# Kernel optimization log

Measured on AMD Instinct MI355X. Metric: run time of the kernel, lower is better.

Reference implementation:

```python
import jax, jax.numpy as jnp
import numpy as np

INV_SQRT2 = 0.7071067811865476


def _quadrature_ops(d):
    # truncated harmonic-oscillator ladder operator: a[n, n+1] = sqrt(n+1)
    a = jnp.diag(jnp.sqrt(jnp.arange(1, d, dtype=jnp.float32)), k=1)
    X0 = (a + a.T) * INV_SQRT2
    P0 = (a - a.T) * INV_SQRT2  # real-valued stand-in for the momentum quadrature
    I = jnp.eye(d, dtype=jnp.float32)
    return I, X0, P0


def setup_inputs() -> dict:
    key = jax.random.key(0)
    ks = jax.random.split(key, 6)
    D, d, w, K = 512, 32, 8, 4
    return {
        "mps_params": jax.random.normal(ks[0], (D, d, D), dtype=jnp.float32),
        "theta": jax.random.normal(ks[1], (1,), dtype=jnp.float32),
        "env_L": jax.random.normal(ks[2], (K, D, w, D), dtype=jnp.float32) * 0.1,
        "env_R": jax.random.normal(ks[3], (K, D, w, D), dtype=jnp.float32) * 0.1,
        "coeffs": jax.random.normal(ks[4], (K, w, w, 5), dtype=jnp.float32),
        "prefactors": jax.random.normal(ks[5], (K,), dtype=jnp.float32),
    }


def reference(mps_params, theta, env_L, env_R, coeffs, prefactors):
    A = mps_params  # [D(left), d(phys), D(right)]
    d = A.shape[1]
    K = prefactors.shape[0]

    # norm_fn: psi.H @ psi for a single-tensor MPS is sum(A^2)
    An = A / jnp.sqrt(jnp.sum(A * A))

    # _get_XandP: quadrature rotation from basis params
    I, X0, P0 = _quadrature_ops(d)
    c, s = jnp.cos(theta[0]), jnp.sin(theta[0])
    X = c * X0 + s * P0
    P = -s * X0 + c * P0

    # dynamic MPO cores: W_k[i,j] = sum_c coeffs[k,i,j,c] * ops[c]
    ops = jnp.stack([I, X, P, X @ X, P @ P])  # [5, d, d]
    W = jnp.einsum('kijc,cab->kijab', coeffs, ops)  # [K, w, w, d, d]

    out = jnp.zeros((), dtype=A.dtype)
    for k in range(K):  # fixed small loop over Hamiltonian constituents
        # T: [L, w, p, r]
        T = jnp.einsum('Lwl,lpr->Lwpr', env_L[k], An)
        # apply MPO core: [L, v, P, r]
        T = jnp.einsum('wvPp,Lwpr->LvPr', W[k], T)
        # close with right env: [L, P, R]
        T = jnp.einsum('LvPr,Rvr->LPR', T, env_R[k])
        out = out + prefactors[k] * jnp.einsum('LPR,LPR->', An, T)
    return out
```

## Files before the change

kernel.cpp:

```cpp
#include <hip/hip_runtime.h>


typedef __attribute__((ext_vector_type(8))) _Float16 f16x8;
typedef __attribute__((ext_vector_type(4))) float f32x4;

__device__ __forceinline__ unsigned short f2h(float f) {
    _Float16 h = (_Float16)f;
    return *(unsigned short*)&h;
}

__device__ __forceinline__ void gload16(const void* g, void* l) {
    __builtin_amdgcn_global_load_lds(
        (const __attribute__((address_space(1))) void*)g,
        (__attribute__((address_space(3))) void*)l, 16, 0, 0);
}

struct GArg {
    const unsigned short* A;
    const unsigned short* B;
    unsigned short* C;
    int kshift;
    long long kextra;
};

__device__ __forceinline__ void stage_tile(
    const GArg& g, int row0, int col0, int kt0,
    short* dstA, short* dstB, int tid)
{
    #pragma unroll
    for (int q = 0; q < 4; ++q) {
        const int c = q * 512 + tid;
        const int r = c >> 3;
        const int gs = (c & 7) ^ (r & 7);
        const int gr = row0 + r;
        const size_t aoff = (size_t)gr * 512 + (size_t)((unsigned)gr >> g.kshift) * g.kextra;
        gload16(g.A + aoff + kt0 + gs * 8, dstA + c * 8);
        gload16(g.B + (size_t)(col0 + r) * 512 + kt0 + gs * 8, dstB + c * 8);
    }
}

__global__ __launch_bounds__(512, 2) void gemm_dual256(int K, GArg g0, GArg g1)
{
    __shared__ short lds[65536];
    const GArg g = blockIdx.z ? g1 : g0;
    const int tid = threadIdx.x;
    const int wid = tid >> 6, lane = tid & 63;
    const int wm = wid >> 2, wn = wid & 3;
    const int lrow = lane & 15, lgrp = lane >> 4;
    const int sx = lrow & 7;
    const int gsw0 = (lgrp ^ sx) * 8, gsw1 = ((lgrp + 4) ^ sx) * 8;

    const int flat = blockIdx.y * 64 + blockIdx.x;
    const int xcd = flat & 7, local = flat >> 3;
    const int col0 = (xcd * 8 + (local & 7)) * 256;
    const int row0 = (local >> 3) * 256;

    const int nt = K >> 6;
    short* A0 = lds;          short* B0 = lds + 16384;
    short* A1 = lds + 32768;  short* B1 = lds + 49152;

    f32x4 acc[8][4] = {};

    stage_tile(g, row0, col0, 0, A0, B0, tid);
    stage_tile(g, row0, col0, 64, A1, B1, tid);
    asm volatile("s_waitcnt vmcnt(8)" ::: "memory");
    __builtin_amdgcn_s_barrier();
    __builtin_amdgcn_sched_barrier(0);

    for (int t = 0; t < nt; ++t) {
        const short* cA = (t & 1) ? A1 : A0;
        const short* cB = (t & 1) ? B1 : B0;
        short* wA = (t & 1) ? A1 : A0;
        short* wB = (t & 1) ? B1 : B0;

        f16x8 bfr[4][2], afr[4][2];
        #pragma unroll
        for (int j = 0; j < 4; ++j) {
            const int R = wn * 64 + j * 16 + lrow;
            bfr[j][0] = *(const f16x8*)&cB[R * 64 + gsw0];
            bfr[j][1] = *(const f16x8*)&cB[R * 64 + gsw1];
        }
        #pragma unroll
        for (int i = 0; i < 4; ++i) {
            const int R = wm * 128 + i * 16 + lrow;
            afr[i][0] = *(const f16x8*)&cA[R * 64 + gsw0];
            afr[i][1] = *(const f16x8*)&cA[R * 64 + gsw1];
        }
        __builtin_amdgcn_s_setprio(1);
        #pragma unroll
        for (int i = 0; i < 4; ++i)
            #pragma unroll
            for (int j = 0; j < 4; ++j) {
                acc[i][j] = __builtin_amdgcn_mfma_f32_16x16x32_f16(afr[i][0], bfr[j][0], acc[i][j], 0, 0, 0);
                acc[i][j] = __builtin_amdgcn_mfma_f32_16x16x32_f16(afr[i][1], bfr[j][1], acc[i][j], 0, 0, 0);
            }
        __builtin_amdgcn_s_setprio(0);
        #pragma unroll
        for (int i = 0; i < 4; ++i) {
            const int R = wm * 128 + (i + 4) * 16 + lrow;
            afr[i][0] = *(const f16x8*)&cA[R * 64 + gsw0];
            afr[i][1] = *(const f16x8*)&cA[R * 64 + gsw1];
        }
        asm volatile("s_waitcnt lgkmcnt(0)" ::: "memory");
        __builtin_amdgcn_sched_barrier(0);
        __builtin_amdgcn_s_barrier();
        __builtin_amdgcn_sched_barrier(0);
        if (t + 2 < nt)
            stage_tile(g, row0, col0, (t + 2) * 64, wA, wB, tid);
        __builtin_amdgcn_s_setprio(1);
        #pragma unroll
        for (int i = 0; i < 4; ++i)
            #pragma unroll
            for (int j = 0; j < 4; ++j) {
                acc[i + 4][j] = __builtin_amdgcn_mfma_f32_16x16x32_f16(afr[i][0], bfr[j][0], acc[i + 4][j], 0, 0, 0);
                acc[i + 4][j] = __builtin_amdgcn_mfma_f32_16x16x32_f16(afr[i][1], bfr[j][1], acc[i + 4][j], 0, 0, 0);
            }
        __builtin_amdgcn_s_setprio(0);
        if (t < nt - 1) {
            if (t + 2 < nt) asm volatile("s_waitcnt vmcnt(8)" ::: "memory");
            else            asm volatile("s_waitcnt vmcnt(0)" ::: "memory");
            __builtin_amdgcn_sched_barrier(0);
            __builtin_amdgcn_s_barrier();
            __builtin_amdgcn_sched_barrier(0);
        }
    }

    const int orow = lgrp * 4, ocol = lrow;
    __syncthreads();
    #pragma unroll
    for (int h = 0; h < 2; ++h) {
        if (wm == h) {
            #pragma unroll
            for (int i = 0; i < 8; ++i)
                #pragma unroll
                for (int j = 0; j < 4; ++j)
                    #pragma unroll
                    for (int q = 0; q < 4; ++q)
                        lds[(i * 16 + orow + q) * 264 + wn * 64 + j * 16 + ocol] =
                            (short)f2h(acc[i][j][q]);
        }
        __syncthreads();
        #pragma unroll
        for (int s2 = 0; s2 < 8; ++s2) {
            const int ch = s2 * 512 + tid;
            const int rr = ch >> 5, c16 = ch & 31;
            *(int4*)(g.C + (size_t)(row0 + h * 128 + rr) * 16384 + col0 + c16 * 8) =
                *(const int4*)&lds[rr * 264 + c16 * 8];
        }
        __syncthreads();
    }
}

__global__ __launch_bounds__(1024) void gemm_g4w(
    const unsigned short* __restrict__ T1, const unsigned short* __restrict__ Yp,
    const float* __restrict__ W2p, float* __restrict__ dacc,
    int Lt8, int zkShift, int BKC)
{
    __shared__ short sh[16384];
    const int tid = threadIdx.x;
    const int wid = tid >> 6, lane = tid & 63;
    const int kidx = blockIdx.x >> zkShift;
    const int kz = (blockIdx.x - (kidx << zkShift)) * BKC;
    const int wr = (wid >> 2) * 64, wc = (wid & 3) * 64;
    const int lrow = lane & 15, kb = (lane >> 4) * 8;

    const int r = tid >> 2, kc = (tid & 3) * 8;
    const int w_ = r >> 5, p_ = r & 31;
    const size_t T1k = (size_t)kidx * Lt8 * 16384;
    const size_t Yk = (size_t)kidx * 4096;
    const size_t aoff = T1k + (size_t)w_ * 16384 + (size_t)p_ * 512;
    const size_t boff = Yk + (size_t)p_ * 16384 + (size_t)w_ * 512;

    f32x4 acc[4][4] = {};

    for (int k0 = 0; k0 < BKC; k0 += 32) {
        const int kk = kz + k0;
        const int lt = kk >> 9, rbase = kk & 511;
        gload16(T1 + aoff + (size_t)lt * 131072 + rbase + kc, sh + tid * 8);
        gload16(Yp + boff + (size_t)lt * 524288 + rbase + kc, sh + 8192 + tid * 8);
        __syncthreads();
        f16x8 a[4], b[4];
        #pragma unroll
        for (int i = 0; i < 4; ++i)
            a[i] = *(const f16x8*)&sh[(wr + i * 16 + lrow) * 32 + kb];
        #pragma unroll
        for (int j = 0; j < 4; ++j)
            b[j] = *(const f16x8*)&sh[8192 + (wc + j * 16 + lrow) * 32 + kb];
        #pragma unroll
        for (int i = 0; i < 4; ++i)
            #pragma unroll
            for (int j = 0; j < 4; ++j)
                acc[i][j] = __builtin_amdgcn_mfma_f32_16x16x32_f16(a[i], b[j], acc[i][j], 0, 0, 0);
        __syncthreads();
    }

    const int orow = (lane >> 4) * 4, ocol = lane & 15;
    const float* Wk = W2p + ((size_t)kidx << 16);
    float s = 0.f;
    #pragma unroll
    for (int j = 0; j < 4; ++j) {
        const int n = wc + j * 16 + ocol;
        const float* wrow = Wk + (size_t)n * 256 + wr + orow;
        #pragma unroll
        for (int i = 0; i < 4; ++i) {
            float4 wv = *(const float4*)(wrow + i * 16);
            s += wv.x * acc[i][j][0] + wv.y * acc[i][j][1]
               + wv.z * acc[i][j][2] + wv.w * acc[i][j][3];
        }
    }
    __syncthreads();
    float* red = (float*)sh;
    red[tid] = s;
    __syncthreads();
    for (int st = 512; st > 0; st >>= 1) {
        if (tid < st) red[tid] += red[tid + st];
        __syncthreads();
    }
    if (tid == 0) atomicAdd(dacc, red[0]);
}

__global__ __launch_bounds__(256) void cast_sumsq(
    const float* __restrict__ in, unsigned short* __restrict__ out,
    long long n4, float* __restrict__ sumsq)
{
    float p = 0.f;
    for (long long i = (long long)blockIdx.x * blockDim.x + threadIdx.x; i < n4;
         i += (long long)gridDim.x * blockDim.x) {
        float4 v = ((const float4*)in)[i];
        p += v.x * v.x + v.y * v.y + v.z * v.z + v.w * v.w;
        union { unsigned short s[4]; uint2 d; } o;
        o.s[0] = f2h(v.x); o.s[1] = f2h(v.y); o.s[2] = f2h(v.z); o.s[3] = f2h(v.w);
        ((uint2*)out)[i] = o.d;
    }
    __shared__ float sh[256];
    sh[threadIdx.x] = p;
    __syncthreads();
    for (int s = 128; s > 0; s >>= 1) {
        if (threadIdx.x < s) sh[threadIdx.x] += sh[threadIdx.x + s];
        __syncthreads();
    }
    if (threadIdx.x == 0) atomicAdd(sumsq, sh[0]);
}

__global__ void cast_kernel(const float* __restrict__ in, unsigned short* __restrict__ out,
                            long long n4)
{
    for (long long i = (long long)blockIdx.x * blockDim.x + threadIdx.x; i < n4;
         i += (long long)gridDim.x * blockDim.x) {
        float4 v = ((const float4*)in)[i];
        union { unsigned short s[4]; uint2 d; } o;
        o.s[0] = f2h(v.x); o.s[1] = f2h(v.y); o.s[2] = f2h(v.z); o.s[3] = f2h(v.w);
        ((uint2*)out)[i] = o.d;
    }
}

__global__ void transpose_cast(const float* __restrict__ in, unsigned short* __restrict__ out,
                               int R, int C, long long in_stride, long long out_stride)
{
    __shared__ float tile[32][33];
    in += (long long)blockIdx.z * in_stride;
    out += (long long)blockIdx.z * out_stride;
    int c0 = blockIdx.x * 32, r0 = blockIdx.y * 32;
    int tx = threadIdx.x, ty = threadIdx.y;
    #pragma unroll
    for (int i = 0; i < 4; ++i)
        tile[ty + i * 8][tx] = in[(size_t)(r0 + ty + i * 8) * C + c0 + tx];
    __syncthreads();
    #pragma unroll
    for (int i = 0; i < 4; ++i)
        out[(size_t)(c0 + ty + i * 8) * R + r0 + tx] = f2h(tile[tx][ty + i * 8]);
}

__global__ void build_ops(const float* __restrict__ theta, float* __restrict__ ops)
{
    __shared__ float X[32][32], Pm[32][32];
    int i = threadIdx.y, j = threadIdx.x;
    float c = cosf(theta[0]), s = sinf(theta[0]);
    float aij = (j == i + 1) ? sqrtf((float)j) : 0.f;
    float aji = (i == j + 1) ? sqrtf((float)i) : 0.f;
    const float inv = 0.70710678118654752440f;
    float x0 = (aij + aji) * inv;
    float p0 = (aij - aji) * inv;
    X[i][j] = c * x0 + s * p0;
    Pm[i][j] = -s * x0 + c * p0;
    __syncthreads();
    float xx = 0.f, pp = 0.f;
    #pragma unroll
    for (int m = 0; m < 32; ++m) {
        xx += X[i][m] * X[m][j];
        pp += Pm[i][m] * Pm[m][j];
    }
    ops[0 * 1024 + i * 32 + j] = (i == j) ? 1.f : 0.f;
    ops[1 * 1024 + i * 32 + j] = X[i][j];
    ops[2 * 1024 + i * 32 + j] = Pm[i][j];
    ops[3 * 1024 + i * 32 + j] = xx;
    ops[4 * 1024 + i * 32 + j] = pp;
}

__global__ void build_w(const float* __restrict__ coeffs, const float* __restrict__ ops,
                        const float* __restrict__ pref, float* __restrict__ W2)
{
    int b = blockIdx.x;
    int k = b >> 6, w = (b >> 3) & 7, v = b & 7;
    int P = threadIdx.y, p = threadIdx.x;
    const float* cf = coeffs + ((k * 8 + w) * 8 + v) * 5;
    float acc = 0.f;
    #pragma unroll
    for (int c = 0; c < 5; ++c) acc += cf[c] * ops[c * 1024 + P * 32 + p];
    W2[(size_t)k * 65536 + (v * 32 + P) * 256 + (w * 32 + p)] = acc * pref[k];
}

__global__ void finalize_kernel(const float* __restrict__ dacc, const float* __restrict__ sumsq,
                                float* __restrict__ out)
{
    if (threadIdx.x == 0) out[0] = dacc[0] / sumsq[0];
}

extern "C" void kernel_launch(void* const* d_in, const int* in_sizes, int n_in,
                              void* d_out, int out_size, void* d_ws, size_t ws_size,
                              hipStream_t stream)
{
    const float* A      = (const float*)d_in[0];
    const float* theta  = (const float*)d_in[1];
    const float* envL   = (const float*)d_in[2];
    const float* envR   = (const float*)d_in[3];
    const float* coeffs = (const float*)d_in[4];
    const float* pref   = (const float*)d_in[5];
    float* out = (float*)d_out;

    char* ws = (char*)d_ws;
    float* sumsq = (float*)ws;
    float* dacc  = (float*)(ws + 4);
    float* ops   = (float*)(ws + 64);
    float* W2    = (float*)(ws + (32 << 10));
    unsigned short* envLh  = (unsigned short*)(ws + (4ull << 20));
    unsigned short* Ah     = (unsigned short*)(ws + (21ull << 20));
    unsigned short* Ath    = (unsigned short*)(ws + (38ull << 20));
    unsigned short* envRth = (unsigned short*)(ws + (55ull << 20));
    const size_t big0 = 72ull << 20;

    int Lt = 64;
    while (Lt > 8) {
        size_t need = big0 + 2ull * (size_t)Lt * (1ull << 20);
        if (need <= ws_size) break;
        Lt >>= 1;
    }
    unsigned short* T1 = (unsigned short*)(ws + big0);
    unsigned short* Yp = T1 + (size_t)Lt * 524288;

    const int Lt8 = Lt * 8;
    const int kshiftA = __builtin_ctz(Lt8);
    const long long kextraA = 2097152LL - (long long)Lt8 * 512;
    const int KT = Lt * 512;
    int BKC = KT / 64; if (BKC < 128) BKC = 128;
    const int zk = KT / BKC;
    const int zkShift = __builtin_ctz(zk);

    hipMemsetAsync(ws, 0, 64, stream);

    cast_sumsq<<<1024, 256, 0, stream>>>(A, Ah, 2097152LL, sumsq);
    build_ops<<<1, dim3(32, 32), 0, stream>>>(theta, ops);
    build_w<<<256, dim3(32, 32), 0, stream>>>(coeffs, ops, pref, W2);
    cast_kernel<<<2048, 256, 0, stream>>>(envL, envLh, 2097152LL);
    transpose_cast<<<dim3(512, 16, 1), dim3(32, 8), 0, stream>>>(A, Ath, 512, 16384, 0, 0);
    transpose_cast<<<dim3(128, 16, 4), dim3(32, 8), 0, stream>>>(envR, envRth, 512, 4096,
                                                                 2097152LL, 2097152LL);

    const int ntiles = 512 / Lt;
    for (int t = 0; t < ntiles; ++t) {
        GArg g0, g1;
        g0.A = envLh + (size_t)t * Lt8 * 512; g0.B = Ath; g0.C = T1;
        g0.kshift = kshiftA; g0.kextra = kextraA;
        g1.A = Ah + (size_t)t * Lt * 16384; g1.B = envRth; g1.C = Yp;
        g1.kshift = 30; g1.kextra = 0;
        gemm_dual256<<<dim3(64, (Lt * 32) / 256, 2), 512, 0, stream>>>(512, g0, g1);
        gemm_g4w<<<dim3(4 * zk), 1024, 0, stream>>>(T1, Yp, W2, dacc, Lt8, zkShift, BKC);
    }
    finalize_kernel<<<1, 64, 0, stream>>>(dacc, sumsq, out);
}
```

Before: 1.042 ms.

## Split GEMM K-tile into half-slabs with four-phase interleaved load/MFMA pipeline

Restructures the 256x256 GEMM main loop so each 64-wide K tile is stored as two 32-wide half-slabs per operand. Global-to-LDS loads are issued in quarter-sized chunks between four MFMA phases, each separated by barriers, instead of one bulk stage per tile. The LDS swizzle changes to match the 32-wide slab layout. Launch bounds drop from 2 to 1 block per CU, which allows more registers but reduces occupancy, and the extra barriers per tile add synchronisation cost.

Result: slower. 1.080 ms (+3.7%).

```diff
diff --git a/kernel.cpp b/kernel.cpp
--- a/kernel.cpp
+++ b/kernel.cpp
@@ -23,23 +23,54 @@
     long long kextra;
 };
 
-__device__ __forceinline__ void stage_tile(
-    const GArg& g, int row0, int col0, int kt0,
-    short* dstA, short* dstB, int tid)
-{
-    #pragma unroll
-    for (int q = 0; q < 4; ++q) {
-        const int c = q * 512 + tid;
-        const int r = c >> 3;
-        const int gs = (c & 7) ^ (r & 7);
-        const int gr = row0 + r;
-        const size_t aoff = (size_t)gr * 512 + (size_t)((unsigned)gr >> g.kshift) * g.kextra;
-        gload16(g.A + aoff + kt0 + gs * 8, dstA + c * 8);
-        gload16(g.B + (size_t)(col0 + r) * 512 + kt0 + gs * 8, dstB + c * 8);
-    }
-}
-
-__global__ __launch_bounds__(512, 2) void gemm_dual256(int K, GArg g0, GArg g1)
+__device__ __forceinline__ void stage_half(
+    const GArg& g, short* lds, int row0, int col0, int tid,
+    int tt, int kh, int isB)
+{
+    short* dst = lds + (tt & 1) * 32768 + isB * 16384 + kh * 8192;
+    const unsigned short* src = isB ? g.B : g.A;
+    #pragma unroll
+    for (int q = 0; q < 2; ++q) {
+        const int s = q * 512 + tid;
+        const int row = s >> 2;
+        const int kgs = (s & 3) ^ ((row >> 1) & 3);
+        size_t off;
+        if (isB) {
+            off = (size_t)(col0 + row) * 512 + tt * 64 + kh * 32 + kgs * 8;
+        } else {
+            const int gr = row0 + row;
+            off = (size_t)gr * 512 + (size_t)((unsigned)gr >> g.kshift) * g.kextra
+                + tt * 64 + kh * 32 + kgs * 8;
+        }
+        gload16(src + off, dst + s * 8);
+    }
+}
+
+#define PHASE_SYNC_IN() do { \
+    __builtin_amdgcn_sched_barrier(0); \
+    __builtin_amdgcn_s_barrier(); \
+    asm volatile("s_waitcnt lgkmcnt(0)" ::: "memory"); \
+    __builtin_amdgcn_sched_barrier(0); \
+} while (0)
+
+#define PHASE_SYNC_OUT() do { \
+    __builtin_amdgcn_sched_barrier(0); \
+    __builtin_amdgcn_s_barrier(); \
+    __builtin_amdgcn_sched_barrier(0); \
+} while (0)
+
+#define MFMA16(base) do { \
+    __builtin_amdgcn_s_setprio(1); \
+    _Pragma("unroll") \
+    for (int ii = 0; ii < 4; ++ii) \
+        _Pragma("unroll") \
+        for (int j = 0; j < 4; ++j) \
+            acc[(base) + ii][j] = __builtin_amdgcn_mfma_f32_16x16x32_f16( \
+                afr[ii], bfr[j], acc[(base) + ii][j], 0, 0, 0); \
+    __builtin_amdgcn_s_setprio(0); \
+} while (0)
+
+__global__ __launch_bounds__(512, 1) void gemm_dual256(int K, GArg g0, GArg g1)
 {
     __shared__ short lds[65536];
     const GArg g = blockIdx.z ? g1 : g0;
@@ -47,8 +78,7 @@
     const int wid = tid >> 6, lane = tid & 63;
     const int wm = wid >> 2, wn = wid & 3;
     const int lrow = lane & 15, lgrp = lane >> 4;
-    const int sx = lrow & 7;
-    const int gsw0 = (lgrp ^ sx) * 8, gsw1 = ((lgrp + 4) ^ sx) * 8;
+    const int rdoff = lrow * 32 + (lgrp ^ ((lrow >> 1) & 3)) * 8;
 
     const int flat = blockIdx.y * 64 + blockIdx.x;
     const int xcd = flat & 7, local = flat >> 3;
@@ -56,73 +86,66 @@
     const int row0 = (local >> 3) * 256;
 
     const int nt = K >> 6;
-    short* A0 = lds;          short* B0 = lds + 16384;
-    short* A1 = lds + 32768;  short* B1 = lds + 49152;
 
     f32x4 acc[8][4] = {};
 
-    stage_tile(g, row0, col0, 0, A0, B0, tid);
-    stage_tile(g, row0, col0, 64, A1, B1, tid);
-    asm volatile("s_waitcnt vmcnt(8)" ::: "memory");
+    stage_half(g, lds, row0, col0, tid, 0, 0, 0);
+    stage_half(g, lds, row0, col0, tid, 0, 0, 1);
+    stage_half(g, lds, row0, col0, tid, 0, 1, 0);
+    stage_half(g, lds, row0, col0, tid, 0, 1, 1);
+    stage_half(g, lds, row0, col0, tid, 1, 0, 0);
+    stage_half(g, lds, row0, col0, tid, 1, 0, 1);
+    asm volatile("s_waitcnt vmcnt(4)" ::: "memory");
     __builtin_amdgcn_s_barrier();
     __builtin_amdgcn_sched_barrier(0);
 
     for (int t = 0; t < nt; ++t) {
-        const short* cA = (t & 1) ? A1 : A0;
-        const short* cB = (t & 1) ? B1 : B0;
-        short* wA = (t & 1) ? A1 : A0;
-        short* wB = (t & 1) ? B1 : B0;
-
-        f16x8 bfr[4][2], afr[4][2];
-        #pragma unroll
-        for (int j = 0; j < 4; ++j) {
-            const int R = wn * 64 + j * 16 + lrow;
-            bfr[j][0] = *(const f16x8*)&cB[R * 64 + gsw0];
-            bfr[j][1] = *(const f16x8*)&cB[R * 64 + gsw1];
-        }
-        #pragma unroll
-        for (int i = 0; i < 4; ++i) {
-            const int R = wm * 128 + i * 16 + lrow;
-            afr[i][0] = *(const f16x8*)&cA[R * 64 + gsw0];
-            afr[i][1] = *(const f16x8*)&cA[R * 64 + gsw1];
-        }
-        __builtin_amdgcn_s_setprio(1);
-        #pragma unroll
-        for (int i = 0; i < 4; ++i)
-            #pragma unroll
-            for (int j = 0; j < 4; ++j) {
-                acc[i][j] = __builtin_amdgcn_mfma_f32_16x16x32_f16(afr[i][0], bfr[j][0], acc[i][j], 0, 0, 0);
-                acc[i][j] = __builtin_amdgcn_mfma_f32_16x16x32_f16(afr[i][1], bfr[j][1], acc[i][j], 0, 0, 0);
-            }
-        __builtin_amdgcn_s_setprio(0);
-        #pragma unroll
-        for (int i = 0; i < 4; ++i) {
-            const int R = wm * 128 + (i + 4) * 16 + lrow;
-            afr[i][0] = *(const f16x8*)&cA[R * 64 + gsw0];
-            afr[i][1] = *(const f16x8*)&cA[R * 64 + gsw1];
-        }
-        asm volatile("s_waitcnt lgkmcnt(0)" ::: "memory");
+        const short* aslab0 = lds + (t & 1) * 32768;
+        const short* aslab1 = aslab0 + 8192;
+        const short* bslab0 = aslab0 + 16384;
+        const short* bslab1 = bslab0 + 8192;
+        f16x8 afr[4], bfr[4];
+
+        #pragma unroll
+        for (int j = 0; j < 4; ++j)
+            bfr[j] = *(const f16x8*)(bslab0 + (wn * 64 + j * 16) * 32 + rdoff);
+        #pragma unroll
+        for (int ii = 0; ii < 4; ++ii)
+            afr[ii] = *(const f16x8*)(aslab0 + (wm * 128 + ii * 16) * 32 + rdoff);
+        if (t + 1 < nt) stage_half(g, lds, row0, col0, tid, t + 1, 1, 0);
+        PHASE_SYNC_IN();
+        MFMA16(0);
+        PHASE_SYNC_OUT();
+
+        #pragma unroll
+        for (int ii = 0; ii < 4; ++ii)
+            afr[ii] = *(const f16x8*)(aslab0 + (wm * 128 + 64 + ii * 16) * 32 + rdoff);
+        if (t + 1 < nt) stage_half(g, lds, row0, col0, tid, t + 1, 1, 1);
+        PHASE_SYNC_IN();
+        MFMA16(4);
+        PHASE_SYNC_OUT();
+
+        #pragma unroll
+        for (int j = 0; j < 4; ++j)
+            bfr[j] = *(const f16x8*)(bslab1 + (wn * 64 + j * 16) * 32 + rdoff);
+        #pragma unroll
+        for (int ii = 0; ii < 4; ++ii)
+            afr[ii] = *(const f16x8*)(aslab1 + (wm * 128 + ii * 16) * 32 + rdoff);
+        if (t + 2 < nt) stage_half(g, lds, row0, col0, tid, t + 2, 0, 0);
+        PHASE_SYNC_IN();
+        MFMA16(0);
+        PHASE_SYNC_OUT();
+
+        #pragma unroll
+        for (int ii = 0; ii < 4; ++ii)
+            afr[ii] = *(const f16x8*)(aslab1 + (wm * 128 + 64 + ii * 16) * 32 + rdoff);
+        if (t + 2 < nt) stage_half(g, lds, row0, col0, tid, t + 2, 0, 1);
+        PHASE_SYNC_IN();
+        MFMA16(4);
         __builtin_amdgcn_sched_barrier(0);
-        __builtin_amdgcn_s_barrier();
-        __builtin_amdgcn_sched_barrier(0);
-        if (t + 2 < nt)
-            stage_tile(g, row0, col0, (t + 2) * 64, wA, wB, tid);
-        __builtin_amdgcn_s_setprio(1);
-        #pragma unroll
-        for (int i = 0; i < 4; ++i)
-            #pragma unroll
-            for (int j = 0; j < 4; ++j) {
-                acc[i + 4][j] = __builtin_amdgcn_mfma_f32_16x16x32_f16(afr[i][0], bfr[j][0], acc[i + 4][j], 0, 0, 0);
-                acc[i + 4][j] = __builtin_amdgcn_mfma_f32_16x16x32_f16(afr[i][1], bfr[j][1], acc[i + 4][j], 0, 0, 0);
-            }
-        __builtin_amdgcn_s_setprio(0);
-        if (t < nt - 1) {
-            if (t + 2 < nt) asm volatile("s_waitcnt vmcnt(8)" ::: "memory");
-            else            asm volatile("s_waitcnt vmcnt(0)" ::: "memory");
-            __builtin_amdgcn_sched_barrier(0);
-            __builtin_amdgcn_s_barrier();
-            __builtin_amdgcn_sched_barrier(0);
-        }
+        if (t + 2 < nt) asm volatile("s_waitcnt vmcnt(4)" ::: "memory");
+        else            asm volatile("s_waitcnt vmcnt(0)" ::: "memory");
+        PHASE_SYNC_OUT();
     }
 
     const int orow = lgrp * 4, ocol = lrow;
```

## Make dual GEMM blocks persistent over four row tiles with streamed epilogue

Applied to the files above, without the earlier changes.

Each block of the dual fp16 GEMM now walks four consecutive 256-row tiles against the same column tile, with one continuous double-buffered K pipeline across tile boundaries. After each tile it writes the results through a small dedicated LDS staging area in 32-row chunks, while the next tile's loads are already in flight. This cuts block launch and prologue/epilogue stalls and reuses B tiles in cache. In exchange occupancy drops to one block per CU with more LDS, grid size falls by four, and the minimum Lt is raised to 32, which needs a larger workspace.

New measurement: 1.023 ms. Within noise of the previous version (-1.8%).

```diff
diff --git a/kernel.cpp b/kernel.cpp
--- a/kernel.cpp
+++ b/kernel.cpp
@@ -24,7 +24,7 @@
 };
 
 __device__ __forceinline__ void stage_tile(
-    const GArg& g, int row0, int col0, int kt0,
+    const GArg& g, int srow0, int col0, int kt0,
     short* dstA, short* dstB, int tid)
 {
     #pragma unroll
@@ -32,16 +32,16 @@
         const int c = q * 512 + tid;
         const int r = c >> 3;
         const int gs = (c & 7) ^ (r & 7);
-        const int gr = row0 + r;
+        const int gr = srow0 + r;
         const size_t aoff = (size_t)gr * 512 + (size_t)((unsigned)gr >> g.kshift) * g.kextra;
         gload16(g.A + aoff + kt0 + gs * 8, dstA + c * 8);
         gload16(g.B + (size_t)(col0 + r) * 512 + kt0 + gs * 8, dstB + c * 8);
     }
 }
 
-__global__ __launch_bounds__(512, 2) void gemm_dual256(int K, GArg g0, GArg g1)
-{
-    __shared__ short lds[65536];
+__global__ __launch_bounds__(512, 1) void gemm_dual_mega(int K, GArg g0, GArg g1)
+{
+    __shared__ short lds[74240];
     const GArg g = blockIdx.z ? g1 : g0;
     const int tid = threadIdx.x;
     const int wid = tid >> 6, lane = tid & 63;
@@ -50,28 +50,30 @@
     const int sx = lrow & 7;
     const int gsw0 = (lgrp ^ sx) * 8, gsw1 = ((lgrp + 4) ^ sx) * 8;
 
-    const int flat = blockIdx.y * 64 + blockIdx.x;
-    const int xcd = flat & 7, local = flat >> 3;
-    const int col0 = (xcd * 8 + (local & 7)) * 256;
-    const int row0 = (local >> 3) * 256;
-
-    const int nt = K >> 6;
+    const int xcd = blockIdx.x & 7, loc = blockIdx.x >> 3;
+    const int col0 = (xcd * 8 + loc) * 256;
+    const int row_base = blockIdx.y * 1024;
+
     short* A0 = lds;          short* B0 = lds + 16384;
     short* A1 = lds + 32768;  short* B1 = lds + 49152;
+    short* repk = lds + 65536;
+
+    const int nt = K >> 6;
+    const int NT = nt * 4;
 
     f32x4 acc[8][4] = {};
 
-    stage_tile(g, row0, col0, 0, A0, B0, tid);
-    stage_tile(g, row0, col0, 64, A1, B1, tid);
+    stage_tile(g, row_base, col0, 0, A0, B0, tid);
+    stage_tile(g, row_base, col0, 64, A1, B1, tid);
     asm volatile("s_waitcnt vmcnt(8)" ::: "memory");
     __builtin_amdgcn_s_barrier();
     __builtin_amdgcn_sched_barrier(0);
 
-    for (int t = 0; t < nt; ++t) {
-        const short* cA = (t & 1) ? A1 : A0;
-        const short* cB = (t & 1) ? B1 : B0;
-        short* wA = (t & 1) ? A1 : A0;
-        short* wB = (t & 1) ? B1 : B0;
+    for (int it = 0; it < NT; ++it) {
+        const short* cA = (it & 1) ? A1 : A0;
+        const short* cB = (it & 1) ? B1 : B0;
+        short* wA = (it & 1) ? A1 : A0;
+        short* wB = (it & 1) ? B1 : B0;
 
         f16x8 bfr[4][2], afr[4][2];
         #pragma unroll
@@ -105,8 +107,10 @@
         __builtin_amdgcn_sched_barrier(0);
         __builtin_amdgcn_s_barrier();
         __builtin_amdgcn_sched_barrier(0);
-        if (t + 2 < nt)
-            stage_tile(g, row0, col0, (t + 2) * 64, wA, wB, tid);
+        if (it + 2 < NT) {
+            const int it2 = it + 2;
+            stage_tile(g, row_base + (it2 >> 3) * 256, col0, (it2 & 7) * 64, wA, wB, tid);
+        }
         __builtin_amdgcn_s_setprio(1);
         #pragma unroll
         for (int i = 0; i < 4; ++i)
@@ -116,38 +120,47 @@
                 acc[i + 4][j] = __builtin_amdgcn_mfma_f32_16x16x32_f16(afr[i][1], bfr[j][1], acc[i + 4][j], 0, 0, 0);
             }
         __builtin_amdgcn_s_setprio(0);
-        if (t < nt - 1) {
-            if (t + 2 < nt) asm volatile("s_waitcnt vmcnt(8)" ::: "memory");
-            else            asm volatile("s_waitcnt vmcnt(0)" ::: "memory");
-            __builtin_amdgcn_sched_barrier(0);
-            __builtin_amdgcn_s_barrier();
-            __builtin_amdgcn_sched_barrier(0);
-        }
-    }
-
-    const int orow = lgrp * 4, ocol = lrow;
-    __syncthreads();
-    #pragma unroll
-    for (int h = 0; h < 2; ++h) {
-        if (wm == h) {
+        __builtin_amdgcn_sched_barrier(0);
+        if (it + 2 < NT) asm volatile("s_waitcnt vmcnt(8)" ::: "memory");
+        else             asm volatile("s_waitcnt vmcnt(0)" ::: "memory");
+        __builtin_amdgcn_sched_barrier(0);
+        __builtin_amdgcn_s_barrier();
+        __builtin_amdgcn_sched_barrier(0);
+
+        if ((it & 7) == 7) {
+            const int row0 = row_base + (it >> 3) * 256;
+            const int orow = lgrp * 4, ocol = lrow;
+            #pragma unroll
+            for (int c8 = 0; c8 < 8; ++c8) {
+                if (wm == (c8 >> 2)) {
+                    const int ib = (c8 & 3) * 2;
+                    #pragma unroll
+                    for (int di = 0; di < 2; ++di)
+                        #pragma unroll
+                        for (int j = 0; j < 4; ++j)
+                            #pragma unroll
+                            for (int q = 0; q < 4; ++q)
+                                repk[(di * 16 + orow + q) * 272 + wn * 64 + j * 16 + ocol] =
+                                    (short)f2h(acc[ib + di][j][q]);
+                }
+                asm volatile("s_waitcnt lgkmcnt(0)" ::: "memory");
+                __builtin_amdgcn_s_barrier();
+                #pragma unroll
+                for (int s2 = 0; s2 < 2; ++s2) {
+                    const int idx = s2 * 512 + tid;
+                    const int rr = idx >> 5, cc = idx & 31;
+                    *(int4*)(g.C + (size_t)(row0 + c8 * 32 + rr) * 16384 + col0 + cc * 8) =
+                        *(const int4*)&repk[rr * 272 + cc * 8];
+                }
+                asm volatile("s_waitcnt lgkmcnt(0)" ::: "memory");
+                __builtin_amdgcn_s_barrier();
+            }
             #pragma unroll
             for (int i = 0; i < 8; ++i)
                 #pragma unroll
                 for (int j = 0; j < 4; ++j)
-                    #pragma unroll
-                    for (int q = 0; q < 4; ++q)
-                        lds[(i * 16 + orow + q) * 264 + wn * 64 + j * 16 + ocol] =
-                            (short)f2h(acc[i][j][q]);
-        }
-        __syncthreads();
-        #pragma unroll
-        for (int s2 = 0; s2 < 8; ++s2) {
-            const int ch = s2 * 512 + tid;
-            const int rr = ch >> 5, c16 = ch & 31;
-            *(int4*)(g.C + (size_t)(row0 + h * 128 + rr) * 16384 + col0 + c16 * 8) =
-                *(const int4*)&lds[rr * 264 + c16 * 8];
-        }
-        __syncthreads();
+                    acc[i][j] = (f32x4){0.f, 0.f, 0.f, 0.f};
+        }
     }
 }
 
@@ -340,7 +353,7 @@
     const size_t big0 = 72ull << 20;
 
     int Lt = 64;
-    while (Lt > 8) {
+    while (Lt > 32) {
         size_t need = big0 + 2ull * (size_t)Lt * (1ull << 20);
         if (need <= ws_size) break;
         Lt >>= 1;
@@ -373,7 +386,7 @@
         g0.kshift = kshiftA; g0.kextra = kextraA;
         g1.A = Ah + (size_t)t * Lt * 16384; g1.B = envRth; g1.C = Yp;
         g1.kshift = 30; g1.kextra = 0;
-        gemm_dual256<<<dim3(64, (Lt * 32) / 256, 2), 512, 0, stream>>>(512, g0, g1);
+        gemm_dual_mega<<<dim3(64, (Lt * 32) / 1024, 2), 512, 0, stream>>>(512, g0, g1);
         gemm_g4w<<<dim3(4 * zk), 1024, 0, stream>>>(T1, Yp, W2, dacc, Lt8, zkShift, BKC);
     }
     finalize_kernel<<<1, 64, 0, stream>>>(dacc, sumsq, out);
```
